# Kernel optimization log

Hardware: AMD Instinct MI355X
Metric: run time of the kernel (lower is better)

Reference implementation:

```python
import jax, jax.numpy as jnp
import numpy as np

B, F, D, C, K = 131072, 32, 16, 64, 8  # batch, features, qsvt degree, classes, KAN grid
CLIP = 1.0 - 1e-6


def setup_inputs() -> dict:
    key = jax.random.key(0)
    ks = jax.random.split(key, 7)
    return {
        "X": jax.random.normal(ks[0], (B, F), jnp.float32),
        "qsvt_phases": 0.1 * jax.random.normal(ks[1], (D,), jnp.float32),
        "lcu_weights": jax.random.uniform(ks[2], (F, D), jnp.float32),
        "sum_scale": jnp.ones((F,), jnp.float32) + 0.1 * jax.random.normal(ks[3], (F,), jnp.float32),
        "sum_bias": 0.1 * jax.random.normal(ks[4], (F,), jnp.float32),
        "kan_coeff": jax.random.normal(ks[5], (C, F, K), jnp.float32) / np.sqrt(F * K),
        "kan_bias": jnp.zeros((C,), jnp.float32),
    }


def reference(X, qsvt_phases, lcu_weights, sum_scale, sum_bias, kan_coeff, kan_bias):
    # QSVT: Chebyshev-with-phases polynomial features of each scalar input,
    # vectorized over (batch, feature) instead of the original Python loops.
    degree = qsvt_phases.shape[0]
    grid = kan_coeff.shape[-1]
    theta = jnp.arccos(jnp.clip(X, -CLIP, CLIP))                  # [B,F]
    kd = jnp.arange(1, degree + 1, dtype=X.dtype)                 # [D]
    qsvt_vecs = jnp.cos(theta[..., None] * kd + qsvt_phases)      # [B,F,D]
    # LCU block: normalized linear combination over the degree axis -> scalar per (b,f)
    lcu = jnp.sum(qsvt_vecs * lcu_weights, axis=-1) / (
        jnp.sum(jnp.abs(lcu_weights), axis=-1) + 1e-6)            # [B,F]
    # QuantumSumBlock (one per feature): per-feature affine + tanh squash
    feat = jnp.tanh(sum_scale * lcu + sum_bias)                   # [B,F]
    # KAN layer: Chebyshev basis expansion then per-(class,feature,basis) coefficients
    t2 = jnp.arccos(jnp.clip(feat, -CLIP, CLIP))                  # [B,F]
    kk = jnp.arange(grid, dtype=X.dtype)                          # [K]
    basis = jnp.cos(t2[..., None] * kk)                           # [B,F,K]
    return jnp.einsum('bfk,cfk->bc', basis, kan_coeff) + kan_bias  # [B,C]
```

## Files before the change

### kernel.cpp

```cpp
#include <hip/hip_runtime.h>

#define F 32
#define Dd 16
#define C 64
#define Kk 8
#define CLIPV (1.0f - 1e-6f)
#define CHUNKS 528
#define TABSTRIDE 36
#define TAB_FLOATS (F * TABSTRIDE)
#define TAB_BYTES (TAB_FLOATS * 4)
#define NBLK 1024
#define MT 2
#define K2 2.8853900817779268f

typedef short v8s __attribute__((ext_vector_type(8)));
typedef float v4f __attribute__((ext_vector_type(4)));
typedef float v2f __attribute__((ext_vector_type(2)));

static __device__ inline unsigned cvtpk(float lo, float hi) {
    unsigned r;
    asm("v_cvt_pk_bf16_f32 %0, %1, %2" : "=v"(r) : "v"(lo), "v"(hi));
    return r;
}

__global__ void qkan_prep(const float* __restrict__ phases,
                          const float* __restrict__ lcu_w,
                          const float* __restrict__ sscale,
                          const float* __restrict__ sbias,
                          float* __restrict__ ws) {
    const int idx = threadIdx.x;
    if (idx < F * Dd) {
        const int f = idx >> 4, d = idx & 15;
        float asum = 0.f;
        for (int dd = 0; dd < Dd; ++dd) asum += fabsf(lcu_w[f * Dd + dd]);
        const float sc = K2 * sscale[f] / (asum + 1e-6f);
        float sp, cp;
        sincosf(phases[d], &sp, &cp);
        const float wv = lcu_w[f * Dd + d];
        ws[f * TABSTRIDE + 2 * d]     = sc * wv * cp;
        ws[f * TABSTRIDE + 2 * d + 1] = -sc * wv * sp;
        if (d == 0) ws[f * TABSTRIDE + 32] = K2 * sbias[f];
    }
}

template <bool WS>
__global__ __launch_bounds__(256, 4) void qkan_kernel(
    const float* __restrict__ X,
    const float* __restrict__ phases,
    const float* __restrict__ lcu_w,
    const float* __restrict__ sscale,
    const float* __restrict__ sbias,
    const float* __restrict__ coeff,
    const float* __restrict__ kbias,
    const float* __restrict__ tab,
    float* __restrict__ out)
{
    __shared__ unsigned short s_basis[F * CHUNKS];
    __shared__ float s_tab[WS ? 4 : TAB_FLOATS];

    const int tid = threadIdx.x;
    const int lane = tid & 63;
    const int wu = __builtin_amdgcn_readfirstlane(tid >> 6);
    const int h = lane >> 4;
    const int r16 = lane & 15;

    if (!WS) {
        for (int idx = tid; idx < F * Dd; idx += 256) {
            const int f = idx >> 4, d = idx & 15;
            float asum = 0.f;
#pragma unroll
            for (int dd = 0; dd < Dd; ++dd) asum += fabsf(lcu_w[f * Dd + dd]);
            const float sc = K2 * sscale[f] / (asum + 1e-6f);
            float sp, cp;
            sincosf(phases[d], &sp, &cp);
            const float wv = lcu_w[f * Dd + d];
            s_tab[f * TABSTRIDE + 2 * d]     = sc * wv * cp;
            s_tab[f * TABSTRIDE + 2 * d + 1] = -sc * wv * sp;
            if (d == 0) s_tab[f * TABSTRIDE + 32] = K2 * sbias[f];
        }
        __syncthreads();
    }

    v8s Bfr[8];
    const int cidx = wu * 16 + r16;
#pragma unroll
    for (int q = 0; q < 8; ++q) {
        const int f = 4 * q + h;
        const float* gp = coeff + ((size_t)(cidx * F + f) * Kk);
        const float4 g0 = *reinterpret_cast<const float4*>(gp);
        const float4 g1 = *reinterpret_cast<const float4*>(gp + 4);
        union { unsigned u[4]; v8s v; } bb;
        bb.u[0] = cvtpk(g0.x, g0.y);
        bb.u[1] = cvtpk(g0.z, g0.w);
        bb.u[2] = cvtpk(g1.x, g1.y);
        bb.u[3] = cvtpk(g1.z, g1.w);
        Bfr[q] = bb.v;
    }
    const float biasreg = kbias[cidx];

    for (int mt = 0; mt < MT; ++mt) {
        const int row_base = (blockIdx.x * MT + mt) * 64;
        if (mt) __syncthreads();

        {
            const float* xr = X + (size_t)(row_base + lane) * F + wu * 8;
            const float4 xa = *reinterpret_cast<const float4*>(xr);
            const float4 xb = *reinterpret_cast<const float4*>(xr + 4);
            const float xv[8] = {xa.x, xa.y, xa.z, xa.w, xb.x, xb.y, xb.z, xb.w};
#pragma unroll
            for (int fl = 0; fl < 8; ++fl) {
                const int f = wu * 8 + fl;
                const float* tfp = WS ? (tab + f * TABSTRIDE) : (s_tab + f * TABSTRIDE);
                const v2f* tf2 = reinterpret_cast<const v2f*>(tfp);
                const float fb = tfp[32];
                const float x = fminf(fmaxf(xv[fl], -CLIPV), CLIPV);
                const float s1 = sqrtf(fmaxf(__builtin_fmaf(-x, x, 1.f), 0.f));
                const float tx = x + x;
                const v2f tx2 = {tx, tx};
                v2f w = {0.f, 0.f}, wp = {0.f, 0.f};
#pragma unroll
                for (int j = 15; j >= 0; --j) {
                    const v2f wn = (tf2[j] - wp) + tx2 * w;
                    wp = w;
                    w = wn;
                }
                float z = fb - wp.x;
                z = __builtin_fmaf(x, w.x, z);
                z = __builtin_fmaf(s1, w.y, z);
                float e;
                asm("v_exp_f32 %0, %1" : "=v"(e) : "v"(z));
                const float rr = __builtin_amdgcn_rcpf(e + 1.f);
                const float t = __builtin_fmaf(-2.f, rr, 1.f);
                const float t2 = t + t;
                const float b1 = t;
                const float b2 = t2 * b1 - 1.f;
                const float b3 = t2 * b2 - b1;
                const float b4 = t2 * b3 - b2;
                const float b5 = t2 * b4 - b3;
                const float b6 = t2 * b5 - b4;
                const float b7 = t2 * b6 - b5;
                uint4 pk;
                pk.x = cvtpk(1.f, b1);
                pk.y = cvtpk(b2, b3);
                pk.z = cvtpk(b4, b5);
                pk.w = cvtpk(b6, b7);
                *reinterpret_cast<uint4*>(&s_basis[f * CHUNKS + lane * 8]) = pk;
            }
        }
        __syncthreads();

        {
#pragma unroll
            for (int t = 0; t < 4; ++t) {
                v4f acc = {0.f, 0.f, 0.f, 0.f};
#pragma unroll
                for (int q = 0; q < 8; ++q) {
                    const v8s a = *reinterpret_cast<const v8s*>(
                        &s_basis[(4 * q + h) * CHUNKS + (t * 16 + r16) * 8]);
                    acc = __builtin_amdgcn_mfma_f32_16x16x32_bf16(a, Bfr[q], acc, 0, 0, 0);
                }
                const int row0 = row_base + t * 16 + h * 4;
#pragma unroll
                for (int i = 0; i < 4; ++i) {
                    out[(size_t)(row0 + i) * C + cidx] = acc[i] + biasreg;
                }
            }
        }
    }
}

extern "C" void kernel_launch(void* const* d_in, const int* in_sizes, int n_in,
                              void* d_out, int out_size, void* d_ws, size_t ws_size,
                              hipStream_t stream) {
    const float* X  = (const float*)d_in[0];
    const float* ph = (const float*)d_in[1];
    const float* lw = (const float*)d_in[2];
    const float* ss = (const float*)d_in[3];
    const float* sb = (const float*)d_in[4];
    const float* kc = (const float*)d_in[5];
    const float* kb = (const float*)d_in[6];
    float* out = (float*)d_out;

    if (d_ws != nullptr && ws_size >= (size_t)TAB_BYTES) {
        float* ws = (float*)d_ws;
        qkan_prep<<<dim3(1), dim3(512), 0, stream>>>(ph, lw, ss, sb, ws);
        qkan_kernel<true><<<dim3(NBLK), dim3(256), 0, stream>>>(
            X, ph, lw, ss, sb, kc, kb, (const float*)ws, out);
    } else {
        qkan_kernel<false><<<dim3(NBLK), dim3(256), 0, stream>>>(
            X, ph, lw, ss, sb, kc, kb, nullptr, out);
    }
}
```

Before: 30.52 us.

## Drop separate prep kernel, compute table per block and prefetch X rows early

Removes the single-block prep kernel launch and always builds the LCU/phase table in shared memory inside each block, switching to fast __sincosf. Both row tiles of X are loaded at kernel start, so their global latency overlaps the table setup and coefficient loads. This saves one launch and its serialization, at the cost of redundant per-block table computation and more live registers.

```diff
diff --git a/kernel.cpp b/kernel.cpp
--- a/kernel.cpp
+++ b/kernel.cpp
@@ -7,8 +7,6 @@
 #define CLIPV (1.0f - 1e-6f)
 #define CHUNKS 528
 #define TABSTRIDE 36
-#define TAB_FLOATS (F * TABSTRIDE)
-#define TAB_BYTES (TAB_FLOATS * 4)
 #define NBLK 1024
 #define MT 2
 #define K2 2.8853900817779268f
@@ -23,27 +21,6 @@
     return r;
 }
 
-__global__ void qkan_prep(const float* __restrict__ phases,
-                          const float* __restrict__ lcu_w,
-                          const float* __restrict__ sscale,
-                          const float* __restrict__ sbias,
-                          float* __restrict__ ws) {
-    const int idx = threadIdx.x;
-    if (idx < F * Dd) {
-        const int f = idx >> 4, d = idx & 15;
-        float asum = 0.f;
-        for (int dd = 0; dd < Dd; ++dd) asum += fabsf(lcu_w[f * Dd + dd]);
-        const float sc = K2 * sscale[f] / (asum + 1e-6f);
-        float sp, cp;
-        sincosf(phases[d], &sp, &cp);
-        const float wv = lcu_w[f * Dd + d];
-        ws[f * TABSTRIDE + 2 * d]     = sc * wv * cp;
-        ws[f * TABSTRIDE + 2 * d + 1] = -sc * wv * sp;
-        if (d == 0) ws[f * TABSTRIDE + 32] = K2 * sbias[f];
-    }
-}
-
-template <bool WS>
 __global__ __launch_bounds__(256, 4) void qkan_kernel(
     const float* __restrict__ X,
     const float* __restrict__ phases,
@@ -52,11 +29,10 @@
     const float* __restrict__ sbias,
     const float* __restrict__ coeff,
     const float* __restrict__ kbias,
-    const float* __restrict__ tab,
     float* __restrict__ out)
 {
     __shared__ unsigned short s_basis[F * CHUNKS];
-    __shared__ float s_tab[WS ? 4 : TAB_FLOATS];
+    __shared__ float s_tab[F * TABSTRIDE];
 
     const int tid = threadIdx.x;
     const int lane = tid & 63;
@@ -64,21 +40,26 @@
     const int h = lane >> 4;
     const int r16 = lane & 15;
 
-    if (!WS) {
-        for (int idx = tid; idx < F * Dd; idx += 256) {
-            const int f = idx >> 4, d = idx & 15;
-            float asum = 0.f;
+    const int rb0 = blockIdx.x * (MT * 64);
+    const float* xr0 = X + (size_t)(rb0 + lane) * F + wu * 8;
+    const float4 xa0 = *reinterpret_cast<const float4*>(xr0);
+    const float4 xb0 = *reinterpret_cast<const float4*>(xr0 + 4);
+    const float* xr1 = xr0 + 64 * F;
+    const float4 xa1 = *reinterpret_cast<const float4*>(xr1);
+    const float4 xb1 = *reinterpret_cast<const float4*>(xr1 + 4);
+
+    for (int idx = tid; idx < F * Dd; idx += 256) {
+        const int f = idx >> 4, d = idx & 15;
+        float asum = 0.f;
 #pragma unroll
-            for (int dd = 0; dd < Dd; ++dd) asum += fabsf(lcu_w[f * Dd + dd]);
-            const float sc = K2 * sscale[f] / (asum + 1e-6f);
-            float sp, cp;
-            sincosf(phases[d], &sp, &cp);
-            const float wv = lcu_w[f * Dd + d];
-            s_tab[f * TABSTRIDE + 2 * d]     = sc * wv * cp;
-            s_tab[f * TABSTRIDE + 2 * d + 1] = -sc * wv * sp;
-            if (d == 0) s_tab[f * TABSTRIDE + 32] = K2 * sbias[f];
-        }
-        __syncthreads();
+        for (int dd = 0; dd < Dd; ++dd) asum += fabsf(lcu_w[f * Dd + dd]);
+        const float sc = K2 * sscale[f] / (asum + 1e-6f);
+        float sp, cp;
+        __sincosf(phases[d], &sp, &cp);
+        const float wv = lcu_w[f * Dd + d];
+        s_tab[f * TABSTRIDE + 2 * d]     = sc * wv * cp;
+        s_tab[f * TABSTRIDE + 2 * d + 1] = -sc * wv * sp;
+        if (d == 0) s_tab[f * TABSTRIDE + 32] = K2 * sbias[f];
     }
 
     v8s Bfr[8];
@@ -98,19 +79,20 @@
     }
     const float biasreg = kbias[cidx];
 
+    __syncthreads();
+
     for (int mt = 0; mt < MT; ++mt) {
-        const int row_base = (blockIdx.x * MT + mt) * 64;
+        const int row_base = rb0 + mt * 64;
         if (mt) __syncthreads();
 
         {
-            const float* xr = X + (size_t)(row_base + lane) * F + wu * 8;
-            const float4 xa = *reinterpret_cast<const float4*>(xr);
-            const float4 xb = *reinterpret_cast<const float4*>(xr + 4);
+            const float4 xa = mt ? xa1 : xa0;
+            const float4 xb = mt ? xb1 : xb0;
             const float xv[8] = {xa.x, xa.y, xa.z, xa.w, xb.x, xb.y, xb.z, xb.w};
 #pragma unroll
             for (int fl = 0; fl < 8; ++fl) {
                 const int f = wu * 8 + fl;
-                const float* tfp = WS ? (tab + f * TABSTRIDE) : (s_tab + f * TABSTRIDE);
+                const float* tfp = s_tab + f * TABSTRIDE;
                 const v2f* tf2 = reinterpret_cast<const v2f*>(tfp);
                 const float fb = tfp[32];
                 const float x = fminf(fmaxf(xv[fl], -CLIPV), CLIPV);
@@ -180,14 +162,5 @@
     const float* kc = (const float*)d_in[5];
     const float* kb = (const float*)d_in[6];
     float* out = (float*)d_out;
-
-    if (d_ws != nullptr && ws_size >= (size_t)TAB_BYTES) {
-        float* ws = (float*)d_ws;
-        qkan_prep<<<dim3(1), dim3(512), 0, stream>>>(ph, lw, ss, sb, ws);
-        qkan_kernel<true><<<dim3(NBLK), dim3(256), 0, stream>>>(
-            X, ph, lw, ss, sb, kc, kb, (const float*)ws, out);
-    } else {
-        qkan_kernel<false><<<dim3(NBLK), dim3(256), 0, stream>>>(
-            X, ph, lw, ss, sb, kc, kb, nullptr, out);
-    }
+    qkan_kernel<<<dim3(NBLK), dim3(256), 0, stream>>>(X, ph, lw, ss, sb, kc, kb, out);
 }
```

Measured after the change: 29.43 us. 3.6% less time.
